# Performance work log

Measured on AMD Instinct MI355X. Metric: run time of the kernel, lower is better.

Reference implementation:

```python
import jax, jax.numpy as jnp
import numpy as np

N, E, B, D = 50000, 800000, 250, 128
EPS = 1e-5


def setup_inputs() -> dict:
    key = jax.random.key(0)
    ks = jax.random.split(key, 12)
    x = jax.random.normal(ks[0], (N, D), jnp.float32)
    w = jax.random.uniform(ks[1], (E, 4), jnp.float32)
    src = jax.random.randint(ks[2], (E,), 0, N)
    dst = jax.random.randint(ks[3], (E,), 0, N)
    graph_ids = jnp.sort(jax.random.randint(ks[4], (N,), 0, B))
    s = 1.0 / np.sqrt(D)
    W1 = jax.random.normal(ks[5], (D, D), jnp.float32) * s
    W2 = jax.random.normal(ks[6], (D, D), jnp.float32) * s
    W3 = jax.random.normal(ks[7], (D, D), jnp.float32) * s
    ln1_g = jnp.ones((D,), jnp.float32)
    ln1_b = jnp.zeros((D,), jnp.float32)
    ln2_g = jnp.ones((D,), jnp.float32)
    ln2_b = jnp.zeros((D,), jnp.float32)
    return dict(x=x, w=w, W1=W1, W2=W2, W3=W3, ln1_g=ln1_g, ln1_b=ln1_b,
                ln2_g=ln2_g, ln2_b=ln2_b, src=src, dst=dst, graph_ids=graph_ids)


def _layernorm(h, g, b):
    mu = jnp.mean(h, axis=-1, keepdims=True)
    var = jnp.mean(jnp.square(h - mu), axis=-1, keepdims=True)
    return (h - mu) * jax.lax.rsqrt(var + EPS) * g + b


def reference(x, w, W1, W2, W3, ln1_g, ln1_b, ln2_g, ln2_b, src, dst, graph_ids):
    # edge feature [E,Fe] -> scalar edge weight [E] (mean over feature dim)
    w_s = jnp.mean(w, axis=-1)
    ones_e = jnp.ones((E,), x.dtype)
    # DGL norm='both': unweighted degrees, clamped to >= 1
    out_deg = jnp.clip(jax.ops.segment_sum(ones_e, src, num_segments=N), 1.0)
    in_deg = jnp.clip(jax.ops.segment_sum(ones_e, dst, num_segments=N), 1.0)
    out_norm = jax.lax.rsqrt(out_deg)[:, None]  # [N,1]
    in_norm = jax.lax.rsqrt(in_deg)[:, None]    # [N,1]

    def gconv(h, W):
        m = (h * out_norm)[src] * w_s[:, None]                 # [E,D] gather-mul
        agg = jax.ops.segment_sum(m, dst, num_segments=N)      # [N,D] scatter-add
        return (agg * in_norm) @ W                              # [N,D_out]

    h = _layernorm(jax.nn.relu(gconv(x, W1)), ln1_g, ln1_b)
    h = _layernorm(jax.nn.relu(gconv(h, W2)), ln2_g, ln2_b)
    h = gconv(h, W3)
    # per-graph segmented sum readout -> [B, D]
    return jax.ops.segment_sum(h, graph_ids, num_segments=B)
```

## Files before the change

### kernel.cpp

```cpp
#include <hip/hip_runtime.h>

#define D 128
#define RS 16
#define NBMAX 1024
constexpr float EPS = 1e-5f;

typedef short bf16x8 __attribute__((ext_vector_type(8)));
typedef float f32x4 __attribute__((ext_vector_type(4)));

__device__ __forceinline__ uint f2bf(float f) {
  union { float f; uint u; } v; v.f = f;
  return (v.u + 0x7fffu + ((v.u >> 16) & 1u)) >> 16;
}
__device__ __forceinline__ float bflo(uint u) {
  union { uint u; float f; } v; v.u = u << 16; return v.f;
}
__device__ __forceinline__ float bfhi(uint u) {
  union { uint u; float f; } v; v.u = u & 0xffff0000u; return v.f;
}

__device__ __forceinline__ int lower_bound(const int* __restrict__ a, int n, int key) {
  int lo = 0, hi = n;
  while (lo < hi) { int m = (lo + hi) >> 1; if (a[m] < key) lo = m + 1; else hi = m; }
  return lo;
}

__global__ __launch_bounds__(256) void k_pre(
    const int* __restrict__ src, const int* __restrict__ dst,
    int* __restrict__ ocnt, int* __restrict__ btot, int E, int nb, int ebA,
    const float4* __restrict__ x, uint4* __restrict__ xb, int n8, int cb,
    const float* __restrict__ W1, const float* __restrict__ W2,
    const float* __restrict__ W3, ushort* __restrict__ Wf) {
  __shared__ int hloc[NBMAX];
  int bid = blockIdx.x;
  int tid = threadIdx.x;
  if (bid < ebA) {
    for (int j = tid; j < nb; j += 256) hloc[j] = 0;
    __syncthreads();
    int e0 = bid * 4096;
#pragma unroll 4
    for (int it = 0; it < 16; ++it) {
      int e = e0 + it * 256 + tid;
      if (e < E) {
        atomicAdd(&ocnt[src[e]], 1);
        atomicAdd(&hloc[dst[e] >> 6], 1);
      }
    }
    __syncthreads();
    for (int j = tid; j < nb; j += 256) {
      int c = hloc[j];
      if (c) atomicAdd(&btot[j], c);
    }
  } else if (bid < ebA + cb) {
    int i = (bid - ebA) * 256 + tid;
    if (i < n8) {
      float4 p = x[i * 2], q = x[i * 2 + 1];
      uint4 o;
      o.x = f2bf(p.x) | (f2bf(p.y) << 16);
      o.y = f2bf(p.z) | (f2bf(p.w) << 16);
      o.z = f2bf(q.x) | (f2bf(q.y) << 16);
      o.w = f2bf(q.z) | (f2bf(q.w) << 16);
      xb[i] = o;
    }
  } else {
    int t4 = (bid - ebA - cb) * 256 + tid;
    if (t4 < 3 * 2048) {
      const float* Wsrc = (t4 < 2048) ? W1 : (t4 < 4096) ? W2 : W3;
      int t = t4 & 2047;
      int lane = t & 63;
      int frag = t >> 6;
      int ks = frag >> 3, ct = frag & 7;
      int col = ct * 16 + (lane & 15);
      int kb = ks * 32 + (lane >> 4) * 8;
      uint p[8];
#pragma unroll
      for (int j = 0; j < 8; ++j) p[j] = f2bf(Wsrc[(kb + j) * D + col]);
      uint4 o;
      o.x = p[0] | (p[1] << 16);
      o.y = p[2] | (p[3] << 16);
      o.z = p[4] | (p[5] << 16);
      o.w = p[6] | (p[7] << 16);
      *(uint4*)(Wf + (size_t)t4 * 8) = o;
    }
  }
}

__global__ void k_onorm(const int* __restrict__ ocnt, float* __restrict__ outn, int N) {
  int n = blockIdx.x * 256 + threadIdx.x;
  if (n < N) outn[n] = rsqrtf(fmaxf((float)ocnt[n], 1.0f));
}

__global__ __launch_bounds__(1024) void k_bbase(const int* __restrict__ btot,
                                                int* __restrict__ bb,
                                                int* __restrict__ rowptr,
                                                int nb, int E, int N) {
  __shared__ int part[1024];
  int t = threadIdx.x;
  int v = (t < nb) ? btot[t] : 0;
  part[t] = v;
  __syncthreads();
  for (int off = 1; off < 1024; off <<= 1) {
    int u = (t >= off) ? part[t - off] : 0;
    __syncthreads();
    part[t] += u;
    __syncthreads();
  }
  if (t < nb) bb[t] = part[t] - v;
  if (t == 0) { bb[nb] = E; rowptr[N] = E; }
}

__global__ __launch_bounds__(256) void k_bscatter(
    const int* __restrict__ src, const int* __restrict__ dst,
    const float4* __restrict__ w, const float* __restrict__ outn,
    const int* __restrict__ bb, int* __restrict__ bcur,
    unsigned long long* __restrict__ ebuf, int E, int nb) {
  __shared__ int hloc[NBMAX];
  __shared__ int hcur[NBMAX];
  int bid = blockIdx.x, tid = threadIdx.x;
  for (int j = tid; j < nb; j += 256) hloc[j] = 0;
  __syncthreads();
  int e0 = bid * 4096;
#pragma unroll 4
  for (int it = 0; it < 16; ++it) {
    int e = e0 + it * 256 + tid;
    if (e < E) atomicAdd(&hloc[dst[e] >> 6], 1);
  }
  __syncthreads();
  for (int j = tid; j < nb; j += 256) {
    int c = hloc[j];
    hcur[j] = c ? (bb[j] + atomicAdd(&bcur[j], c)) : 0;
  }
  __syncthreads();
#pragma unroll 4
  for (int it = 0; it < 16; ++it) {
    int e = e0 + it * 256 + tid;
    if (e < E) {
      int d = dst[e], s = src[e];
      int pos = atomicAdd(&hcur[d >> 6], 1);
      float4 wv = w[e];
      float coef = (wv.x + wv.y + wv.z + wv.w) * 0.25f * outn[s];
      unsigned long long pk = ((unsigned long long)__float_as_uint(coef) << 32) |
                              ((unsigned long long)(d & 63) << 16) | (uint)s;
      ebuf[pos] = pk;
    }
  }
}

__global__ __launch_bounds__(256) void k_bplace(
    const unsigned long long* __restrict__ ebuf, const int* __restrict__ bb,
    int* __restrict__ rowptr, float* __restrict__ innm,
    unsigned long long* __restrict__ ecsr, int N) {
  __shared__ int c64[64], ex[64], cur[64];
  int b = blockIdx.x, tid = threadIdx.x;
  int base = bb[b];
  int cnt = bb[b + 1] - base;
  if (tid < 64) c64[tid] = 0;
  __syncthreads();
  for (int i = tid; i < cnt; i += 256) {
    unsigned long long v = ebuf[base + i];
    atomicAdd(&c64[(int)((v >> 16) & 63)], 1);
  }
  __syncthreads();
  if (tid < 64) {
    int cv = c64[tid];
    int inc = cv;
#pragma unroll
    for (int off = 1; off < 64; off <<= 1) {
      int u = __shfl_up(inc, off);
      if (tid >= off) inc += u;
    }
    int excl = inc - cv;
    ex[tid] = excl;
    cur[tid] = 0;
    int node = b * 64 + tid;
    if (node < N) {
      rowptr[node] = base + excl;
      innm[node] = rsqrtf(fmaxf((float)cv, 1.0f));
    }
  }
  __syncthreads();
  for (int i = tid; i < cnt; i += 256) {
    unsigned long long v = ebuf[base + i];
    int dl = (int)((v >> 16) & 63);
    int pos = base + ex[dl] + atomicAdd(&cur[dl], 1);
    ecsr[pos] = (v & 0xFFFFFFFF00000000ull) | (v & 0xFFFFull);
  }
}

__global__ __launch_bounds__(64) void k_fused(
    const ushort* __restrict__ h, const int* __restrict__ rowptr,
    const unsigned long long* __restrict__ ecsr,
    const float* __restrict__ innm, const ushort* __restrict__ Wf,
    const float* __restrict__ g, const float* __restrict__ bta,
    void* __restrict__ out, int N, int do_ln) {
  __shared__ float lds[16 * D];
  const int lane = threadIdx.x;
  const int lr = lane & 15, lg = lane >> 4;
  const int row0 = blockIdx.x * 16;
  const int row = row0 + lr;
  const bool valid = row < N;

  int beg = 0, end = 0;
  float sc = 0.f;
  if (valid) { beg = rowptr[row]; end = rowptr[row + 1]; sc = innm[row]; }

  float a0[8], a1[8], a2[8], a3[8];
#pragma unroll
  for (int i = 0; i < 8; ++i) { a0[i] = 0; a1[i] = 0; a2[i] = 0; a3[i] = 0; }

#define ACC8(A, q, f)                                          \
  A[0] = fmaf(bflo(q.x), f, A[0]); A[1] = fmaf(bfhi(q.x), f, A[1]); \
  A[2] = fmaf(bflo(q.y), f, A[2]); A[3] = fmaf(bfhi(q.y), f, A[3]); \
  A[4] = fmaf(bflo(q.z), f, A[4]); A[5] = fmaf(bfhi(q.z), f, A[5]); \
  A[6] = fmaf(bflo(q.w), f, A[6]); A[7] = fmaf(bfhi(q.w), f, A[7]);
  for (int j = beg; j < end; ++j) {
    unsigned long long v = ecsr[j];
    float cf = __uint_as_float((uint)(v >> 32));
    int s = (int)(v & 0xFFFFFFFFu);
    const ushort* hp = h + (size_t)s * D + lg * 8;
    uint4 q0 = *(const uint4*)(hp);
    uint4 q1 = *(const uint4*)(hp + 32);
    uint4 q2 = *(const uint4*)(hp + 64);
    uint4 q3 = *(const uint4*)(hp + 96);
    ACC8(a0, q0, cf) ACC8(a1, q1, cf) ACC8(a2, q2, cf) ACC8(a3, q3, cf)
  }
#undef ACC8

  uint4 fa[4];
#define PACK(dst, A)                                             \
  dst.x = f2bf(A[0] * sc) | (f2bf(A[1] * sc) << 16);             \
  dst.y = f2bf(A[2] * sc) | (f2bf(A[3] * sc) << 16);             \
  dst.z = f2bf(A[4] * sc) | (f2bf(A[5] * sc) << 16);             \
  dst.w = f2bf(A[6] * sc) | (f2bf(A[7] * sc) << 16);
  PACK(fa[0], a0) PACK(fa[1], a1) PACK(fa[2], a2) PACK(fa[3], a3)
#undef PACK

  f32x4 acc[8];
#pragma unroll
  for (int ct = 0; ct < 8; ++ct) acc[ct] = (f32x4){0.f, 0.f, 0.f, 0.f};
#pragma unroll
  for (int ks = 0; ks < 4; ++ks) {
    bf16x8 av;
    __builtin_memcpy(&av, &fa[ks], 16);
    const ushort* wp = Wf + ((size_t)(ks * 8) * 64 + lane) * 8;
#pragma unroll
    for (int ct = 0; ct < 8; ++ct) {
      bf16x8 b = *(const bf16x8*)(wp + ct * 512);
      acc[ct] = __builtin_amdgcn_mfma_f32_16x16x32_bf16(av, b, acc[ct], 0, 0, 0);
    }
  }

  if (do_ln) {
    float v[8][4];
#pragma unroll
    for (int ct = 0; ct < 8; ++ct)
#pragma unroll
      for (int j = 0; j < 4; ++j) v[ct][j] = fmaxf(acc[ct][j], 0.f);
    float mu[4], rs[4];
#pragma unroll
    for (int j = 0; j < 4; ++j) {
      float s = 0.f;
#pragma unroll
      for (int ct = 0; ct < 8; ++ct) s += v[ct][j];
#pragma unroll
      for (int off = 1; off < 16; off <<= 1) s += __shfl_xor(s, off);
      mu[j] = s * (1.0f / D);
    }
#pragma unroll
    for (int j = 0; j < 4; ++j) {
      float q = 0.f;
#pragma unroll
      for (int ct = 0; ct < 8; ++ct) {
        v[ct][j] -= mu[j];
        q = fmaf(v[ct][j], v[ct][j], q);
      }
#pragma unroll
      for (int off = 1; off < 16; off <<= 1) q += __shfl_xor(q, off);
      rs[j] = rsqrtf(q * (1.0f / D) + EPS);
    }
    ushort* lp = (ushort*)&lds[0];
#pragma unroll
    for (int ct = 0; ct < 8; ++ct) {
      float gc = g[ct * 16 + lr], bc = bta[ct * 16 + lr];
#pragma unroll
      for (int j = 0; j < 4; ++j)
        lp[(lg * 4 + j) * D + ct * 16 + lr] = (ushort)f2bf(fmaf(v[ct][j] * rs[j], gc, bc));
    }
    __builtin_amdgcn_wave_barrier();
    int r = row0 + (lane >> 2);
    if (r < N) {
      ushort* ob = (ushort*)out + (size_t)row0 * D + lane * 32;
#pragma unroll
      for (int i = 0; i < 4; ++i)
        ((uint4*)ob)[i] = ((const uint4*)(lp + lane * 32))[i];
    }
  } else {
    float* lp = &lds[0];
#pragma unroll
    for (int ct = 0; ct < 8; ++ct)
#pragma unroll
      for (int j = 0; j < 4; ++j)
        lp[(lg * 4 + j) * D + ct * 16 + lr] = acc[ct][j];
    __builtin_amdgcn_wave_barrier();
    int r = row0 + (lane >> 2);
    if (r < N) {
      float* ob = (float*)out + (size_t)row0 * D + lane * 32;
#pragma unroll
      for (int i = 0; i < 8; ++i)
        ((float4*)ob)[i] = ((const float4*)(lp + lane * 32))[i];
    }
  }
}

__global__ __launch_bounds__(128) void k_rpart(
    const float* __restrict__ h, const int* __restrict__ gid,
    float* __restrict__ part, int N) {
  int b = blockIdx.x / RS, s = blockIdx.x % RS;
  int t = threadIdx.x;
  int start = lower_bound(gid, N, b);
  int end = lower_bound(gid, N, b + 1);
  int len = end - start;
  int chunk = (len + RS - 1) / RS;
  int rb = start + s * chunk;
  int re = min(rb + chunk, end);
  float acc = 0.f;
  for (int n = rb; n < re; ++n) acc += h[(size_t)n * D + t];
  part[((size_t)b * RS + s) * D + t] = acc;
}

__global__ __launch_bounds__(128) void k_rsum(
    const float* __restrict__ part, float* __restrict__ out) {
  int b = blockIdx.x;
  int t = threadIdx.x;
  float acc = 0.f;
#pragma unroll
  for (int s = 0; s < RS; ++s) acc += part[((size_t)b * RS + s) * D + t];
  out[(size_t)b * D + t] = acc;
}

extern "C" void kernel_launch(void* const* d_in, const int* in_sizes, int n_in,
                              void* d_out, int out_size, void* d_ws, size_t ws_size,
                              hipStream_t stream) {
  const float* x    = (const float*)d_in[0];
  const float* w    = (const float*)d_in[1];
  const float* W1   = (const float*)d_in[2];
  const float* W2   = (const float*)d_in[3];
  const float* W3   = (const float*)d_in[4];
  const float* ln1g = (const float*)d_in[5];
  const float* ln1b = (const float*)d_in[6];
  const float* ln2g = (const float*)d_in[7];
  const float* ln2b = (const float*)d_in[8];
  const int* src = (const int*)d_in[9];
  const int* dst = (const int*)d_in[10];
  const int* gid = (const int*)d_in[11];
  const int N = in_sizes[0] / D;
  const int E = in_sizes[9];
  const int B = out_size / D;
  float* outp = (float*)d_out;

  float*  h3f  = (float*)d_ws;
  ushort* xb   = (ushort*)(h3f + (size_t)N * D);
  ushort* hb1  = xb + (size_t)N * D;
  ushort* Wf   = hb1 + (size_t)N * D;
  float*  outn = (float*)(Wf + 3 * 2048 * 8);
  float*  innm = outn + N;
  const int nb  = (N + 63) >> 6;
  const int ebA = (E + 4095) / 4096;
  int*    ocnt = (int*)(innm + N);
  int*    btot = ocnt + N;
  int*    bcur = btot + nb;
  int*    rowptr = bcur + nb;
  int*    bb   = rowptr + N + 2;
  unsigned long long* ecsr = (unsigned long long*)(bb + nb + 2);
  float*  part = (float*)(ecsr + E);
  unsigned long long* ebuf = (unsigned long long*)h3f;

  const int mb  = (N + 15) / 16;
  const int n8  = N * D / 8;
  const int cb  = (n8 + 255) / 256;

  hipMemsetAsync(ocnt, 0, sizeof(int) * ((size_t)N + 2 * nb), stream);
  k_pre<<<ebA + cb + 24, 256, 0, stream>>>(src, dst, ocnt, btot, E, nb, ebA,
                                           (const float4*)x, (uint4*)xb, n8, cb,
                                           W1, W2, W3, Wf);
  k_onorm<<<(N + 255) / 256, 256, 0, stream>>>(ocnt, outn, N);
  k_bbase<<<1, 1024, 0, stream>>>(btot, bb, rowptr, nb, E, N);
  k_bscatter<<<ebA, 256, 0, stream>>>(src, dst, (const float4*)w, outn, bb, bcur,
                                      ebuf, E, nb);
  k_bplace<<<nb, 256, 0, stream>>>(ebuf, bb, rowptr, innm, ecsr, N);

  k_fused<<<mb, 64, 0, stream>>>(xb, rowptr, ecsr, innm, Wf,
                                 ln1g, ln1b, hb1, N, 1);
  k_fused<<<mb, 64, 0, stream>>>(hb1, rowptr, ecsr, innm, Wf + 16384,
                                 ln2g, ln2b, xb, N, 1);
  k_fused<<<mb, 64, 0, stream>>>(xb, rowptr, ecsr, innm, Wf + 32768,
                                 nullptr, nullptr, h3f, N, 0);

  k_rpart<<<B * RS, 128, 0, stream>>>(h3f, gid, part, N);
  k_rsum<<<B, 128, 0, stream>>>(part, outp);
}
```

Before: 236.4 us.

## Split edge gather across two waves per row tile and reduce via LDS

The fused gconv kernel now launches two wavefronts per 16-row block. Each wave gathers alternating edges of every row, so the memory-latency-bound gather loop gets twice the waves in flight. The second wave writes its partial accumulators to LDS and exits after a block barrier, and the first wave adds them before the MFMA and layernorm epilogue. This costs an LDS round trip, a __syncthreads, and one idle wave during the matmul and epilogue.

```diff
diff --git a/kernel.cpp b/kernel.cpp
--- a/kernel.cpp
+++ b/kernel.cpp
@@ -7,6 +7,7 @@
 
 typedef short bf16x8 __attribute__((ext_vector_type(8)));
 typedef float f32x4 __attribute__((ext_vector_type(4)));
+typedef unsigned long long u64;
 
 __device__ __forceinline__ uint f2bf(float f) {
   union { float f; uint u; } v; v.f = f;
@@ -113,7 +114,7 @@
     const int* __restrict__ src, const int* __restrict__ dst,
     const float4* __restrict__ w, const float* __restrict__ outn,
     const int* __restrict__ bb, int* __restrict__ bcur,
-    unsigned long long* __restrict__ ebuf, int E, int nb) {
+    u64* __restrict__ ebuf, int E, int nb) {
   __shared__ int hloc[NBMAX];
   __shared__ int hcur[NBMAX];
   int bid = blockIdx.x, tid = threadIdx.x;
@@ -139,17 +140,17 @@
       int pos = atomicAdd(&hcur[d >> 6], 1);
       float4 wv = w[e];
       float coef = (wv.x + wv.y + wv.z + wv.w) * 0.25f * outn[s];
-      unsigned long long pk = ((unsigned long long)__float_as_uint(coef) << 32) |
-                              ((unsigned long long)(d & 63) << 16) | (uint)s;
+      u64 pk = ((u64)__float_as_uint(coef) << 32) |
+               ((u64)(d & 63) << 16) | (uint)s;
       ebuf[pos] = pk;
     }
   }
 }
 
 __global__ __launch_bounds__(256) void k_bplace(
-    const unsigned long long* __restrict__ ebuf, const int* __restrict__ bb,
+    const u64* __restrict__ ebuf, const int* __restrict__ bb,
     int* __restrict__ rowptr, float* __restrict__ innm,
-    unsigned long long* __restrict__ ecsr, int N) {
+    u64* __restrict__ ecsr, int N) {
   __shared__ int c64[64], ex[64], cur[64];
   int b = blockIdx.x, tid = threadIdx.x;
   int base = bb[b];
@@ -157,7 +158,7 @@
   if (tid < 64) c64[tid] = 0;
   __syncthreads();
   for (int i = tid; i < cnt; i += 256) {
-    unsigned long long v = ebuf[base + i];
+    u64 v = ebuf[base + i];
     atomicAdd(&c64[(int)((v >> 16) & 63)], 1);
   }
   __syncthreads();
@@ -180,21 +181,22 @@
   }
   __syncthreads();
   for (int i = tid; i < cnt; i += 256) {
-    unsigned long long v = ebuf[base + i];
+    u64 v = ebuf[base + i];
     int dl = (int)((v >> 16) & 63);
     int pos = base + ex[dl] + atomicAdd(&cur[dl], 1);
     ecsr[pos] = (v & 0xFFFFFFFF00000000ull) | (v & 0xFFFFull);
   }
 }
 
-__global__ __launch_bounds__(64) void k_fused(
+__global__ __launch_bounds__(128) void k_fused(
     const ushort* __restrict__ h, const int* __restrict__ rowptr,
-    const unsigned long long* __restrict__ ecsr,
+    const u64* __restrict__ ecsr,
     const float* __restrict__ innm, const ushort* __restrict__ Wf,
     const float* __restrict__ g, const float* __restrict__ bta,
     void* __restrict__ out, int N, int do_ln) {
   __shared__ float lds[16 * D];
-  const int lane = threadIdx.x;
+  const int lane = threadIdx.x & 63;
+  const int wid = threadIdx.x >> 6;
   const int lr = lane & 15, lg = lane >> 4;
   const int row0 = blockIdx.x * 16;
   const int row = row0 + lr;
@@ -208,23 +210,59 @@
 #pragma unroll
   for (int i = 0; i < 8; ++i) { a0[i] = 0; a1[i] = 0; a2[i] = 0; a3[i] = 0; }
 
-#define ACC8(A, q, f)                                          \
-  A[0] = fmaf(bflo(q.x), f, A[0]); A[1] = fmaf(bfhi(q.x), f, A[1]); \
-  A[2] = fmaf(bflo(q.y), f, A[2]); A[3] = fmaf(bfhi(q.y), f, A[3]); \
-  A[4] = fmaf(bflo(q.z), f, A[4]); A[5] = fmaf(bfhi(q.z), f, A[5]); \
-  A[6] = fmaf(bflo(q.w), f, A[6]); A[7] = fmaf(bfhi(q.w), f, A[7]);
-  for (int j = beg; j < end; ++j) {
-    unsigned long long v = ecsr[j];
-    float cf = __uint_as_float((uint)(v >> 32));
-    int s = (int)(v & 0xFFFFFFFFu);
-    const ushort* hp = h + (size_t)s * D + lg * 8;
-    uint4 q0 = *(const uint4*)(hp);
-    uint4 q1 = *(const uint4*)(hp + 32);
-    uint4 q2 = *(const uint4*)(hp + 64);
-    uint4 q3 = *(const uint4*)(hp + 96);
-    ACC8(a0, q0, cf) ACC8(a1, q1, cf) ACC8(a2, q2, cf) ACC8(a3, q3, cf)
-  }
-#undef ACC8
+#define EDGE(J)                                                  \
+  {                                                              \
+    u64 v = ecsr[J];                                             \
+    float cf = __uint_as_float((uint)(v >> 32));                 \
+    int s = (int)(v & 0xFFFFFFFFu);                              \
+    const ushort* hp = h + (size_t)s * D + lg * 8;               \
+    uint4 q0 = *(const uint4*)(hp);                              \
+    uint4 q1 = *(const uint4*)(hp + 32);                         \
+    uint4 q2 = *(const uint4*)(hp + 64);                         \
+    uint4 q3 = *(const uint4*)(hp + 96);                         \
+    a0[0] = fmaf(bflo(q0.x), cf, a0[0]); a0[1] = fmaf(bfhi(q0.x), cf, a0[1]); \
+    a0[2] = fmaf(bflo(q0.y), cf, a0[2]); a0[3] = fmaf(bfhi(q0.y), cf, a0[3]); \
+    a0[4] = fmaf(bflo(q0.z), cf, a0[4]); a0[5] = fmaf(bfhi(q0.z), cf, a0[5]); \
+    a0[6] = fmaf(bflo(q0.w), cf, a0[6]); a0[7] = fmaf(bfhi(q0.w), cf, a0[7]); \
+    a1[0] = fmaf(bflo(q1.x), cf, a1[0]); a1[1] = fmaf(bfhi(q1.x), cf, a1[1]); \
+    a1[2] = fmaf(bflo(q1.y), cf, a1[2]); a1[3] = fmaf(bfhi(q1.y), cf, a1[3]); \
+    a1[4] = fmaf(bflo(q1.z), cf, a1[4]); a1[5] = fmaf(bfhi(q1.z), cf, a1[5]); \
+    a1[6] = fmaf(bflo(q1.w), cf, a1[6]); a1[7] = fmaf(bfhi(q1.w), cf, a1[7]); \
+    a2[0] = fmaf(bflo(q2.x), cf, a2[0]); a2[1] = fmaf(bfhi(q2.x), cf, a2[1]); \
+    a2[2] = fmaf(bflo(q2.y), cf, a2[2]); a2[3] = fmaf(bfhi(q2.y), cf, a2[3]); \
+    a2[4] = fmaf(bflo(q2.z), cf, a2[4]); a2[5] = fmaf(bfhi(q2.z), cf, a2[5]); \
+    a2[6] = fmaf(bflo(q2.w), cf, a2[6]); a2[7] = fmaf(bfhi(q2.w), cf, a2[7]); \
+    a3[0] = fmaf(bflo(q3.x), cf, a3[0]); a3[1] = fmaf(bfhi(q3.x), cf, a3[1]); \
+    a3[2] = fmaf(bflo(q3.y), cf, a3[2]); a3[3] = fmaf(bfhi(q3.y), cf, a3[3]); \
+    a3[4] = fmaf(bflo(q3.z), cf, a3[4]); a3[5] = fmaf(bfhi(q3.z), cf, a3[5]); \
+    a3[6] = fmaf(bflo(q3.w), cf, a3[6]); a3[7] = fmaf(bfhi(q3.w), cf, a3[7]); \
+  }
+
+  int j = beg + wid;
+  for (; j + 2 < end; j += 4) { EDGE(j) EDGE(j + 2) }
+  if (j < end) EDGE(j)
+#undef EDGE
+
+  if (wid == 1) {
+#pragma unroll
+    for (int i = 0; i < 8; ++i) {
+      lds[i * 64 + lane]        = a0[i];
+      lds[(i + 8) * 64 + lane]  = a1[i];
+      lds[(i + 16) * 64 + lane] = a2[i];
+      lds[(i + 24) * 64 + lane] = a3[i];
+    }
+  }
+  __syncthreads();
+  if (wid == 1) return;
+#pragma unroll
+  for (int i = 0; i < 8; ++i) {
+    a0[i] += lds[i * 64 + lane];
+    a1[i] += lds[(i + 8) * 64 + lane];
+    a2[i] += lds[(i + 16) * 64 + lane];
+    a3[i] += lds[(i + 24) * 64 + lane];
+  }
+  asm volatile("s_waitcnt lgkmcnt(0)" ::: "memory");
+  __builtin_amdgcn_sched_barrier(0);
 
   uint4 fa[4];
 #define PACK(dst, A)                                             \
@@ -255,36 +293,36 @@
 #pragma unroll
     for (int ct = 0; ct < 8; ++ct)
 #pragma unroll
-      for (int j = 0; j < 4; ++j) v[ct][j] = fmaxf(acc[ct][j], 0.f);
+      for (int j2 = 0; j2 < 4; ++j2) v[ct][j2] = fmaxf(acc[ct][j2], 0.f);
     float mu[4], rs[4];
 #pragma unroll
-    for (int j = 0; j < 4; ++j) {
+    for (int j2 = 0; j2 < 4; ++j2) {
       float s = 0.f;
 #pragma unroll
-      for (int ct = 0; ct < 8; ++ct) s += v[ct][j];
+      for (int ct = 0; ct < 8; ++ct) s += v[ct][j2];
 #pragma unroll
       for (int off = 1; off < 16; off <<= 1) s += __shfl_xor(s, off);
-      mu[j] = s * (1.0f / D);
-    }
-#pragma unroll
-    for (int j = 0; j < 4; ++j) {
+      mu[j2] = s * (1.0f / D);
+    }
+#pragma unroll
+    for (int j2 = 0; j2 < 4; ++j2) {
       float q = 0.f;
 #pragma unroll
       for (int ct = 0; ct < 8; ++ct) {
-        v[ct][j] -= mu[j];
-        q = fmaf(v[ct][j], v[ct][j], q);
+        v[ct][j2] -= mu[j2];
+        q = fmaf(v[ct][j2], v[ct][j2], q);
       }
 #pragma unroll
       for (int off = 1; off < 16; off <<= 1) q += __shfl_xor(q, off);
-      rs[j] = rsqrtf(q * (1.0f / D) + EPS);
+      rs[j2] = rsqrtf(q * (1.0f / D) + EPS);
     }
     ushort* lp = (ushort*)&lds[0];
 #pragma unroll
     for (int ct = 0; ct < 8; ++ct) {
       float gc = g[ct * 16 + lr], bc = bta[ct * 16 + lr];
 #pragma unroll
-      for (int j = 0; j < 4; ++j)
-        lp[(lg * 4 + j) * D + ct * 16 + lr] = (ushort)f2bf(fmaf(v[ct][j] * rs[j], gc, bc));
+      for (int j2 = 0; j2 < 4; ++j2)
+        lp[(lg * 4 + j2) * D + ct * 16 + lr] = (ushort)f2bf(fmaf(v[ct][j2] * rs[j2], gc, bc));
     }
     __builtin_amdgcn_wave_barrier();
     int r = row0 + (lane >> 2);
@@ -299,8 +337,8 @@
 #pragma unroll
     for (int ct = 0; ct < 8; ++ct)
 #pragma unroll
-      for (int j = 0; j < 4; ++j)
-        lp[(lg * 4 + j) * D + ct * 16 + lr] = acc[ct][j];
+      for (int j2 = 0; j2 < 4; ++j2)
+        lp[(lg * 4 + j2) * D + ct * 16 + lr] = acc[ct][j2];
     __builtin_amdgcn_wave_barrier();
     int r = row0 + (lane >> 2);
     if (r < N) {
@@ -371,9 +409,9 @@
   int*    bcur = btot + nb;
   int*    rowptr = bcur + nb;
   int*    bb   = rowptr + N + 2;
-  unsigned long long* ecsr = (unsigned long long*)(bb + nb + 2);
+  u64*    ecsr = (u64*)(bb + nb + 2);
   float*  part = (float*)(ecsr + E);
-  unsigned long long* ebuf = (unsigned long long*)h3f;
+  u64*    ebuf = (u64*)h3f;
 
   const int mb  = (N + 15) / 16;
   const int n8  = N * D / 8;
@@ -389,12 +427,12 @@
                                       ebuf, E, nb);
   k_bplace<<<nb, 256, 0, stream>>>(ebuf, bb, rowptr, innm, ecsr, N);
 
-  k_fused<<<mb, 64, 0, stream>>>(xb, rowptr, ecsr, innm, Wf,
-                                 ln1g, ln1b, hb1, N, 1);
-  k_fused<<<mb, 64, 0, stream>>>(hb1, rowptr, ecsr, innm, Wf + 16384,
-                                 ln2g, ln2b, xb, N, 1);
-  k_fused<<<mb, 64, 0, stream>>>(xb, rowptr, ecsr, innm, Wf + 32768,
-                                 nullptr, nullptr, h3f, N, 0);
+  k_fused<<<mb, 128, 0, stream>>>(xb, rowptr, ecsr, innm, Wf,
+                                  ln1g, ln1b, hb1, N, 1);
+  k_fused<<<mb, 128, 0, stream>>>(hb1, rowptr, ecsr, innm, Wf + 16384,
+                                  ln2g, ln2b, xb, N, 1);
+  k_fused<<<mb, 128, 0, stream>>>(xb, rowptr, ecsr, innm, Wf + 32768,
+                                  nullptr, nullptr, h3f, N, 0);
 
   k_rpart<<<B * RS, 128, 0, stream>>>(h3f, gid, part, N);
   k_rsum<<<B, 128, 0, stream>>>(part, outp);
```

Measured after the change: 238.7 us. Within noise of the previous version (+1.0%).
